# Kernel optimization log

Hardware: AMD Instinct MI355X
Metric: run time of the kernel (lower is better)

Reference implementation:

```python
import jax, jax.numpy as jnp
import numpy as np

B, T, D_IN, D_PHYS, H, L, C = 64, 512, 256, 32, 512, 2, 11


def setup_inputs() -> dict:
    key = jax.random.key(0)
    ks = jax.random.split(key, 20)
    def w(k, shape, fan_in):
        return jax.random.normal(k, shape, dtype=jnp.float32) * (1.0 / np.sqrt(fan_in))
    return {
        "main_feats": jax.random.normal(ks[0], (B, T, D_IN), dtype=jnp.float32),
        "phys_feats": jax.random.normal(ks[1], (B, T, D_PHYS), dtype=jnp.float32),
        "mask": jnp.ones((B, T), dtype=jnp.bool_),
        # main_proj
        "Wp": w(ks[2], (H, D_IN), D_IN), "bp": jnp.zeros((H,), jnp.float32),
        # prev-token embedding
        "emb": jax.random.normal(ks[3], (C, H), dtype=jnp.float32),
        # LSTM layer 0 (input 2H) and layer 1 (input H), PyTorch gate order i,f,g,o
        "Wih0": w(ks[4], (4 * H, 2 * H), 2 * H), "Whh0": w(ks[5], (4 * H, H), H),
        "bih0": jnp.zeros((4 * H,), jnp.float32), "bhh0": jnp.zeros((4 * H,), jnp.float32),
        "Wih1": w(ks[6], (4 * H, H), H), "Whh1": w(ks[7], (4 * H, H), H),
        "bih1": jnp.zeros((4 * H,), jnp.float32), "bhh1": jnp.zeros((4 * H,), jnp.float32),
        # head: Linear(H+phys -> H), ReLU, Linear(H -> C)
        "W1": w(ks[8], (H, H + D_PHYS), H + D_PHYS), "b1": jnp.zeros((H,), jnp.float32),
        "W2": w(ks[9], (C, H), H), "b2": jnp.zeros((C,), jnp.float32),
    }


def _lstm_cell(x, h, c, Wih, Whh, bih, bhh):
    g = x @ Wih.T + bih + h @ Whh.T + bhh          # [b, 4H]
    i, f, gg, o = jnp.split(g, 4, axis=-1)          # PyTorch order i,f,g,o
    c2 = jax.nn.sigmoid(f) * c + jax.nn.sigmoid(i) * jnp.tanh(gg)
    h2 = jax.nn.sigmoid(o) * jnp.tanh(c2)
    return h2, c2


def reference(main_feats, phys_feats, mask, Wp, bp, emb,
              Wih0, Whh0, bih0, bhh0, Wih1, Whh1, bih1, bhh1,
              W1, b1, W2, b2):
    b = main_feats.shape[0]
    h = Whh0.shape[1]
    x_main = main_feats @ Wp.T + bp                 # [B,T,H]

    def step(carry, xs):
        h0, c0, h1, c1, prev = carry
        xm, ph = xs                                  # [B,H], [B,phys]
        x = jnp.concatenate([xm, emb[prev]], axis=-1)  # [B,2H]
        h0, c0 = _lstm_cell(x, h0, c0, Wih0, Whh0, bih0, bhh0)
        h1, c1 = _lstm_cell(h0, h1, c1, Wih1, Whh1, bih1, bhh1)
        z = jnp.concatenate([h1, ph], axis=-1)       # [B,H+phys]
        logits = jax.nn.relu(z @ W1.T + b1) @ W2.T + b2  # [B,C]
        prev = jnp.argmax(logits, axis=-1)
        return (h0, c0, h1, c1, prev), logits

    zeros = jnp.zeros((b, h), jnp.float32)
    carry0 = (zeros, zeros, zeros, zeros, jnp.zeros((b,), jnp.int32))
    xs = (x_main.swapaxes(0, 1), phys_feats.swapaxes(0, 1))  # time-major
    _, logits_t = jax.lax.scan(step, carry0, xs)             # [T,B,C]
    logits_all = logits_t.swapaxes(0, 1)                     # [B,T,C]
    attn = jnp.zeros(mask.shape, logits_all.dtype)
    return logits_all, jnp.zeros_like(logits_all), attn
```

## Files before the change

kernel.cpp:

```cpp
#include <hip/hip_runtime.h>

#define Tn   512
#define NWG  256
#define NTH  1024

#define OFF_WCOMB 0
#define OFF_BC0   524288
#define OFF_EMBG  526336
#define OFF_H0T   548864
#define OFF_H1T   (OFF_H0T + 65536)
#define OFF_C0T   (OFF_H1T + 65536)
#define OFF_C1T   (OFF_C0T + 32768)
#define OFF_BAR   (OFF_C1T + 32768)
#define OFF_ARR   (OFF_BAR + 32)
#define OFF_TAG1  (OFF_ARR + 8192)
#define OFF_PTAG  (OFF_TAG1 + 8192)
#define ZERO_END  (OFF_PTAG + 2048)
#define ZERO_WORDS (ZERO_END - OFF_H0T)
#define OFF_PBUF  ZERO_END
#define WS_WORDS  (OFF_PBUF + 704 * 256)

#define OUT_LOGITS_WORDS 360448
#define OUT_TAIL_WORDS   393216

__global__ void k_wcomb(const float* __restrict__ Wih0, const float* __restrict__ Wp,
                        const float* __restrict__ bp, const float* __restrict__ bih0,
                        const float* __restrict__ bhh0, float* __restrict__ ws) {
    int j = blockIdx.x;
    int k = threadIdx.x;
    const float* row = Wih0 + (long)j * 1024;
    float acc = 0.f;
    for (int h = 0; h < 512; ++h) acc = fmaf(row[h], Wp[h * 256 + k], acc);
    ws[OFF_WCOMB + j * 256 + k] = acc;
    __shared__ float s[256];
    s[k] = row[k] * bp[k] + row[256 + k] * bp[256 + k];
    __syncthreads();
    for (int st = 128; st > 0; st >>= 1) { if (k < st) s[k] += s[k + st]; __syncthreads(); }
    if (k == 0) ws[OFF_BC0 + j] = bih0[j] + bhh0[j] + s[0];
}

__global__ void k_embg(const float* __restrict__ emb, const float* __restrict__ Wih0,
                       float* __restrict__ ws) {
    int cls = blockIdx.x >> 3;
    int j = ((blockIdx.x & 7) << 8) + threadIdx.x;
    const float* er = emb + cls * 512;
    const float* wr = Wih0 + (long)j * 1024 + 512;
    float acc = 0.f;
    for (int h = 0; h < 512; ++h) acc = fmaf(er[h], wr[h], acc);
    ws[OFF_EMBG + cls * 2048 + j] = acc;
}

__global__ void k_zero(float* __restrict__ ws) {
    long i = (long)blockIdx.x * blockDim.x + threadIdx.x;
    if (i < ZERO_WORDS) ws[OFF_H0T + i] = 0.f;
}

struct MP {
    const float *mainf, *phys, *Whh0, *Wih1, *Whh1, *bih1, *bhh1, *W1, *b1, *W2, *b2;
    float* ws;
    float* out;
};

__device__ __forceinline__ float sigm(float x) { return 1.f / (1.f + expf(-x)); }

__device__ __forceinline__ void coh_issue16(const float* p, float4& v) {
    asm volatile("global_load_dwordx4 %0, %1, off sc0 sc1" : "=&v"(v) : "v"(p));
}
__device__ __forceinline__ void vm_wait0() {
    asm volatile("s_waitcnt vmcnt(0)" ::: "memory");
}
__device__ __forceinline__ void coh_store(float* p, float v) {
    __hip_atomic_store(p, v, __ATOMIC_RELAXED, __HIP_MEMORY_SCOPE_AGENT);
}

__device__ __forceinline__ void comp_g(const float (*at)[36], const float* wp, int wld, int kA,
                                       int rg, int q, int b4, float* acc) {
    float4 a0 = *(const float4*)&at[(q << 2) + 0][b4 << 2];
    float4 a1 = *(const float4*)&at[(q << 2) + 1][b4 << 2];
    float4 a2 = *(const float4*)&at[(q << 2) + 2][b4 << 2];
    float4 a3 = *(const float4*)&at[(q << 2) + 3][b4 << 2];
#pragma unroll
    for (int jr = 0; jr < 4; ++jr) {
        float4 w4 = *(const float4*)(wp + (long)((rg << 2) + jr) * wld + kA + (q << 2));
        acc[jr * 4 + 0] = fmaf(w4.x, a0.x, acc[jr * 4 + 0]);
        acc[jr * 4 + 0] = fmaf(w4.y, a1.x, acc[jr * 4 + 0]);
        acc[jr * 4 + 0] = fmaf(w4.z, a2.x, acc[jr * 4 + 0]);
        acc[jr * 4 + 0] = fmaf(w4.w, a3.x, acc[jr * 4 + 0]);
        acc[jr * 4 + 1] = fmaf(w4.x, a0.y, acc[jr * 4 + 1]);
        acc[jr * 4 + 1] = fmaf(w4.y, a1.y, acc[jr * 4 + 1]);
        acc[jr * 4 + 1] = fmaf(w4.z, a2.y, acc[jr * 4 + 1]);
        acc[jr * 4 + 1] = fmaf(w4.w, a3.y, acc[jr * 4 + 1]);
        acc[jr * 4 + 2] = fmaf(w4.x, a0.z, acc[jr * 4 + 2]);
        acc[jr * 4 + 2] = fmaf(w4.y, a1.z, acc[jr * 4 + 2]);
        acc[jr * 4 + 2] = fmaf(w4.z, a2.z, acc[jr * 4 + 2]);
        acc[jr * 4 + 2] = fmaf(w4.w, a3.z, acc[jr * 4 + 2]);
        acc[jr * 4 + 3] = fmaf(w4.x, a0.w, acc[jr * 4 + 3]);
        acc[jr * 4 + 3] = fmaf(w4.y, a1.w, acc[jr * 4 + 3]);
        acc[jr * 4 + 3] = fmaf(w4.z, a2.w, acc[jr * 4 + 3]);
        acc[jr * 4 + 3] = fmaf(w4.w, a3.w, acc[jr * 4 + 3]);
    }
}

template <int NCH0>
__device__ void mm_g(const float* a0, long rs0, int km0, int coh0,
                     const float* a1,
                     const float* w0, int wld0, const float* w1,
                     int bq, int tid,
                     float (*aA)[36], float (*aB)[36],
                     float* redw, float* redf) {
    constexpr int NQ0 = (NCH0 + 8) / 2;
    const int b4 = tid & 7, q = (tid >> 3) & 15, rg = (tid >> 7) & 3;
    const int st = tid & 511, sb = tid >> 9;
    float acc[16];
#pragma unroll
    for (int i = 0; i < 16; ++i) acc[i] = 0.f;

    for (int it = 0; it < NQ0; ++it) {
        const int ch = sb ? (NQ0 + it) : it;
        float4 av;
        int km;
        {
            const float* base; int k0, coh;
            if (ch < NCH0) { base = a0; k0 = ch << 6; km = km0; coh = coh0; }
            else           { base = a1; k0 = (ch - NCH0) << 6; km = 1; coh = 1; }
            if (km) {
                const int kk = st >> 3, b4f = st & 7;
                const float* pp = base + ((long)(k0 + kk) << 6) + (bq << 5) + (b4f << 2);
                if (coh) coh_issue16(pp, av); else av = *(const float4*)pp;
            } else {
                const int k4 = st >> 5, bb = st & 31;
                av = *(const float4*)(base + (long)((bq << 5) + bb) * rs0 + k0 + (k4 << 2));
            }
        }
        vm_wait0();
        {
            float (*dst)[36] = sb ? aB : aA;
            if (km) {
                const int kk = st >> 3, b4f = st & 7;
                *(float4*)&dst[kk][b4f << 2] = av;
            } else {
                const int k4 = st >> 5, bb = st & 31;
                dst[(k4 << 2) + 0][bb] = av.x; dst[(k4 << 2) + 1][bb] = av.y;
                dst[(k4 << 2) + 2][bb] = av.z; dst[(k4 << 2) + 3][bb] = av.w;
            }
        }
        __syncthreads();
        if (tid < 512) {
            {
                const int cA = it; const float* wp; int wld, kA;
                if (cA < NCH0) { wp = w0; wld = wld0; kA = cA << 6; }
                else           { wp = w1; wld = 512;  kA = (cA - NCH0) << 6; }
                comp_g(aA, wp, wld, kA, rg, q, b4, acc);
            }
            {
                const int cB = NQ0 + it; const float* wp; int wld, kB;
                if (cB < NCH0) { wp = w0; wld = wld0; kB = cB << 6; }
                else           { wp = w1; wld = 512;  kB = (cB - NCH0) << 6; }
                comp_g(aB, wp, wld, kB, rg, q, b4, acc);
            }
        }
        __syncthreads();
    }
#pragma unroll
    for (int i = 0; i < 16; ++i) {
        acc[i] += __shfl_xor(acc[i], 8);
        acc[i] += __shfl_xor(acc[i], 16);
        acc[i] += __shfl_xor(acc[i], 32);
    }
    const int lane = tid & 63;
    if (tid < 512 && ((tid >> 6) & 1) && lane < 8) {
        float* d = redw + (((rg << 3) + lane) << 4);
#pragma unroll
        for (int i = 0; i < 16; ++i) d[i] = acc[i];
    }
    __syncthreads();
    if (tid < 512 && !((tid >> 6) & 1) && lane < 8) {
        const float* s = redw + (((rg << 3) + lane) << 4);
#pragma unroll
        for (int jr = 0; jr < 4; ++jr)
#pragma unroll
            for (int jb = 0; jb < 4; ++jb)
                redf[((rg << 2) + jr) * 33 + (lane << 2) + jb] = acc[jr * 4 + jb] + s[jr * 4 + jb];
    }
    __syncthreads();
}

__device__ void mm_h(const float* h1, const float* physb, long rsp,
                     const float* W1, int kg, int bq, int tid,
                     float (*aA)[36], float (*aB)[36],
                     float (*hwA)[68], float (*hwB)[68],
                     float* redw, float* redf) {
    const int b4 = tid & 7, q = (tid >> 3) & 15, rg = (tid >> 7) & 3;
    const int st = tid & 511, sb = tid >> 9;
    float acc[4] = {0.f, 0.f, 0.f, 0.f};
    for (int it = 0; it < 5; ++it) {
        const int ch = sb ? (5 + it) : it;
        const bool valid = ch < 9;
        float4 av, wv;
        bool fa = false, fw = false;
        if (valid) {
            if (ch < 8) {
                const int kk = st >> 3, b4f = st & 7;
                coh_issue16(h1 + ((long)((ch << 6) + kk) << 6) + (bq << 5) + (b4f << 2), av);
                fa = true;
            } else {
                const int k4 = st >> 5, bb = st & 31;
                if (k4 < 8) {
                    av = *(const float4*)(physb + (long)((bq << 5) + bb) * rsp + (k4 << 2));
                    fa = true;
                }
            }
            if (st < 64) {
                const int rw = st >> 4, kq = st & 15;
                if (ch < 8 || kq < 8) {
                    const int gcol = (ch < 8) ? ((ch << 6) + (kq << 2)) : (512 + (kq << 2));
                    wv = *(const float4*)(W1 + (long)(kg * 4 + rw) * 544 + gcol);
                    fw = true;
                }
            }
        }
        vm_wait0();
        if (fa) {
            float (*dst)[36] = sb ? aB : aA;
            if (ch < 8) { const int kk = st >> 3, b4f = st & 7; *(float4*)&dst[kk][b4f << 2] = av; }
            else { const int k4 = st >> 5, bb = st & 31;
                   dst[(k4 << 2) + 0][bb] = av.x; dst[(k4 << 2) + 1][bb] = av.y;
                   dst[(k4 << 2) + 2][bb] = av.z; dst[(k4 << 2) + 3][bb] = av.w; }
        }
        if (fw) {
            float (*dw)[68] = sb ? hwB : hwA;
            *(float4*)&dw[st >> 4][(st & 15) << 2] = wv;
        }
        __syncthreads();
        if (tid < 512) {
            {
                float4 a0 = *(const float4*)&aA[(q << 2) + 0][b4 << 2];
                float4 a1v = *(const float4*)&aA[(q << 2) + 1][b4 << 2];
                float4 a2 = *(const float4*)&aA[(q << 2) + 2][b4 << 2];
                float4 a3 = *(const float4*)&aA[(q << 2) + 3][b4 << 2];
                float4 w4 = *(const float4*)&hwA[rg][q << 2];
                acc[0] = fmaf(w4.x, a0.x, acc[0]); acc[0] = fmaf(w4.y, a1v.x, acc[0]);
                acc[0] = fmaf(w4.z, a2.x, acc[0]); acc[0] = fmaf(w4.w, a3.x, acc[0]);
                acc[1] = fmaf(w4.x, a0.y, acc[1]); acc[1] = fmaf(w4.y, a1v.y, acc[1]);
                acc[1] = fmaf(w4.z, a2.y, acc[1]); acc[1] = fmaf(w4.w, a3.y, acc[1]);
                acc[2] = fmaf(w4.x, a0.z, acc[2]); acc[2] = fmaf(w4.y, a1v.z, acc[2]);
                acc[2] = fmaf(w4.z, a2.z, acc[2]); acc[2] = fmaf(w4.w, a3.z, acc[2]);
                acc[3] = fmaf(w4.x, a0.w, acc[3]); acc[3] = fmaf(w4.y, a1v.w, acc[3]);
                acc[3] = fmaf(w4.z, a2.w, acc[3]); acc[3] = fmaf(w4.w, a3.w, acc[3]);
            }
            const int cB = 5 + it;
            const int kc = (cB == 8) ? 32 : 64;
            if (cB < 9 && (q << 2) < kc) {
                float4 a0 = *(const float4*)&aB[(q << 2) + 0][b4 << 2];
                float4 a1v = *(const float4*)&aB[(q << 2) + 1][b4 << 2];
                float4 a2 = *(const float4*)&aB[(q << 2) + 2][b4 << 2];
                float4 a3 = *(const float4*)&aB[(q << 2) + 3][b4 << 2];
                float4 w4 = *(const float4*)&hwB[rg][q << 2];
                acc[0] = fmaf(w4.x, a0.x, acc[0]); acc[0] = fmaf(w4.y, a1v.x, acc[0]);
                acc[0] = fmaf(w4.z, a2.x, acc[0]); acc[0] = fmaf(w4.w, a3.x, acc[0]);
                acc[1] = fmaf(w4.x, a0.y, acc[1]); acc[1] = fmaf(w4.y, a1v.y, acc[1]);
                acc[1] = fmaf(w4.z, a2.y, acc[1]); acc[1] = fmaf(w4.w, a3.y, acc[1]);
                acc[2] = fmaf(w4.x, a0.z, acc[2]); acc[2] = fmaf(w4.y, a1v.z, acc[2]);
                acc[2] = fmaf(w4.z, a2.z, acc[2]); acc[2] = fmaf(w4.w, a3.z, acc[2]);
                acc[3] = fmaf(w4.x, a0.w, acc[3]); acc[3] = fmaf(w4.y, a1v.w, acc[3]);
                acc[3] = fmaf(w4.z, a2.w, acc[3]); acc[3] = fmaf(w4.w, a3.w, acc[3]);
            }
        }
        __syncthreads();
    }
#pragma unroll
    for (int i = 0; i < 4; ++i) {
        acc[i] += __shfl_xor(acc[i], 8);
        acc[i] += __shfl_xor(acc[i], 16);
        acc[i] += __shfl_xor(acc[i], 32);
    }
    const int lane = tid & 63;
    if (tid < 512 && ((tid >> 6) & 1) && lane < 8) {
        float* d = redw + (((rg << 3) + lane) << 4);
#pragma unroll
        for (int i = 0; i < 4; ++i) d[i] = acc[i];
    }
    __syncthreads();
    if (tid < 512 && !((tid >> 6) & 1) && lane < 8) {
        const float* s = redw + (((rg << 3) + lane) << 4);
#pragma unroll
        for (int jb = 0; jb < 4; ++jb)
            redf[rg * 33 + (lane << 2) + jb] = acc[jb] + s[jb];
    }
    __syncthreads();
}

__device__ __forceinline__ void gsync(int* done, int* arr, int w, int gen) {
    vm_wait0();
    __syncthreads();
    const int tid = threadIdx.x;
    if (tid == 0)
        __hip_atomic_store(&arr[w * 32], gen, __ATOMIC_RELAXED, __HIP_MEMORY_SCOPE_AGENT);
    if (w == 0) {
        if (tid < NWG) {
            int v;
            do {
                __builtin_amdgcn_s_sleep(1);
                v = __hip_atomic_load(&arr[tid * 32], __ATOMIC_RELAXED, __HIP_MEMORY_SCOPE_AGENT);
            } while (v < gen);
        }
        __syncthreads();
        if (tid == 0)
            __hip_atomic_store(done, gen, __ATOMIC_RELAXED, __HIP_MEMORY_SCOPE_AGENT);
    } else {
        if (tid == 0) {
            int v;
            do {
                __builtin_amdgcn_s_sleep(2);
                v = __hip_atomic_load(done, __ATOMIC_RELAXED, __HIP_MEMORY_SCOPE_AGENT);
            } while (v < gen);
        }
    }
    __syncthreads();
}

__global__ void __launch_bounds__(NTH, 4) k_main(MP p) {
    float* ws = p.ws;
    const float* bc0v = ws + OFF_BC0;
    const float* embg = ws + OFF_EMBG;
    float* h0T = ws + OFF_H0T;
    float* h1T = ws + OFF_H1T;
    float* c0T = ws + OFF_C0T;
    float* c1T = ws + OFF_C1T;
    float* pbuf = ws + OFF_PBUF;
    int* done = (int*)(ws + OFF_BAR);
    int* arr  = (int*)(ws + OFF_ARR);
    int* tag1 = (int*)(ws + OFF_TAG1);
    int* ptag = (int*)(ws + OFF_PTAG);

    __shared__ float Wc_l[16][256];
    __shared__ float W0_l[16][512];
    __shared__ float Wi1_l[16][512];
    __shared__ float Wh1_l[16][512];
    __shared__ float actA[64][36], actB[64][36];
    __shared__ float hwA[4][68], hwB[4][68];
    __shared__ float redw[512];
    __shared__ float redf[16 * 33];
    __shared__ float rrowS[4][33];
    __shared__ float slog[11];
    __shared__ int prevlS[32];

    const int w = blockIdx.x, tid = threadIdx.x;
    const int kg = w >> 1, bq = w & 1;
    int gen = 0;

    for (int e = tid; e < 4096; e += NTH) {
        int r = e >> 8, c = e & 255;
        int j = (r >> 2) * 512 + kg * 4 + (r & 3);
        Wc_l[r][c] = ws[OFF_WCOMB + (long)j * 256 + c];
    }
    for (int e = tid; e < 8192; e += NTH) {
        int r = e >> 9, c = e & 511;
        int j = (r >> 2) * 512 + kg * 4 + (r & 3);
        W0_l[r][c]  = p.Whh0[(long)j * 512 + c];
        Wi1_l[r][c] = p.Wih1[(long)j * 512 + c];
        Wh1_l[r][c] = p.Whh1[(long)j * 512 + c];
    }
    __syncthreads();

    for (int t = 0; t <= Tn; ++t) {
        const int cur = t & 1, prv = cur ^ 1;

        if (t >= 1) {
            mm_h(h1T + prv * 32768, p.phys + (long)(t - 1) * 32, (long)Tn * 32,
                 p.W1, kg, bq, tid, actA, actB, hwA, hwB, redw, redf);
            if (tid < 128) {
                int rr = tid >> 5, bb = tid & 31;
                float hv = redf[rr * 33 + bb] + p.b1[kg * 4 + rr];
                rrowS[rr][bb] = hv > 0.f ? hv : 0.f;
            }
            __syncthreads();
            if (tid < 352) {
                int bb = tid / 11, cc = tid - bb * 11;
                float s = 0.f;
#pragma unroll
                for (int r = 0; r < 4; ++r)
                    s = fmaf(rrowS[r][bb], p.W2[cc * 512 + kg * 4 + r], s);
                int b = bq * 32 + bb;
                coh_store(&pbuf[(long)(b * 11 + cc) * 128 + kg], s);
            }
            vm_wait0();
            __syncthreads();
            if (tid == 0)
                __hip_atomic_store(&tag1[w * 32], t, __ATOMIC_RELAXED, __HIP_MEMORY_SCOPE_AGENT);

            if (bq == 0 && kg < 64) {
                const int b = kg;
                if (tid < 128) {
                    int v;
                    do {
                        __builtin_amdgcn_s_sleep(1);
                        v = __hip_atomic_load(&tag1[(tid * 2 + (b >> 5)) * 32],
                                              __ATOMIC_RELAXED, __HIP_MEMORY_SCOPE_AGENT);
                    } while (v < t);
                }
                __syncthreads();
                if (tid < 704) {
                    int cc = tid >> 6, kgi = tid & 63;
                    float s = __hip_atomic_load(&pbuf[(long)(b * 11 + cc) * 128 + kgi],
                                                __ATOMIC_RELAXED, __HIP_MEMORY_SCOPE_AGENT)
                            + __hip_atomic_load(&pbuf[(long)(b * 11 + cc) * 128 + kgi + 64],
                                                __ATOMIC_RELAXED, __HIP_MEMORY_SCOPE_AGENT);
#pragma unroll
                    for (int off = 32; off; off >>= 1) s += __shfl_down(s, off);
                    if (kgi == 0) slog[cc] = s + p.b2[cc];
                }
                __syncthreads();
                if (tid == 0) {
                    float best = -3.4e38f; int am = 0;
#pragma unroll
                    for (int cc = 0; cc < 11; ++cc) {
                        float v = slog[cc];
                        p.out[(long)b * (Tn * 11) + (long)(t - 1) * 11 + cc] = v;
                        if (v > best) { best = v; am = cc; }
                    }
                    __hip_atomic_store(&ptag[b * 32], (t << 4) | am,
                                       __ATOMIC_RELAXED, __HIP_MEMORY_SCOPE_AGENT);
                }
            }
        }
        if (t == Tn) break;

        mm_g<4>(p.mainf + (long)t * 256, (long)Tn * 256, 0, 0,
                h0T + prv * 32768, &Wc_l[0][0], 256, &W0_l[0][0],
                bq, tid, actA, actB, redw, redf);
        if (tid < 32) {
            if (t >= 1) {
                int v;
                do {
                    __builtin_amdgcn_s_sleep(1);
                    v = __hip_atomic_load(&ptag[(bq * 32 + tid) * 32],
                                          __ATOMIC_RELAXED, __HIP_MEMORY_SCOPE_AGENT);
                } while ((v >> 4) < t);
                prevlS[tid] = v & 15;
            } else prevlS[tid] = 0;
        }
        __syncthreads();
        if (tid < 512) {
            int rr = tid >> 5, bb = tid & 31;
            int jrow = (rr >> 2) * 512 + kg * 4 + (rr & 3);
            redf[rr * 33 + bb] += bc0v[jrow] + embg[prevlS[bb] * 2048 + jrow];
        }
        __syncthreads();
        if (tid < 128) {
            int jj = tid >> 5, bb = tid & 31;
            int k = kg * 4 + jj, b = bq * 32 + bb;
            float g0 = redf[jj * 33 + bb];
            float g1 = redf[(4 + jj) * 33 + bb];
            float g2 = redf[(8 + jj) * 33 + bb];
            float g3 = redf[(12 + jj) * 33 + bb];
            float ci = c0T[k * 64 + b];
            float cn = sigm(g1) * ci + sigm(g0) * tanhf(g2);
            c0T[k * 64 + b] = cn;
            coh_store(&h0T[cur * 32768 + k * 64 + b], sigm(g3) * tanhf(cn));
        }
        gsync(done, arr, w, ++gen);

        mm_g<8>(h0T + cur * 32768, 0, 1, 1,
                h1T + prv * 32768, &Wi1_l[0][0], 512, &Wh1_l[0][0],
                bq, tid, actA, actB, redw, redf);
        if (tid < 512) {
            int rr = tid >> 5, bb = tid & 31;
            int jrow = (rr >> 2) * 512 + kg * 4 + (rr & 3);
            redf[rr * 33 + bb] += p.bih1[jrow] + p.bhh1[jrow];
        }
        __syncthreads();
        if (tid < 128) {
            int jj = tid >> 5, bb = tid & 31;
            int k = kg * 4 + jj, b = bq * 32 + bb;
            float g0 = redf[jj * 33 + bb];
            float g1 = redf[(4 + jj) * 33 + bb];
            float g2 = redf[(8 + jj) * 33 + bb];
            float g3 = redf[(12 + jj) * 33 + bb];
            float ci = c1T[k * 64 + b];
            float cn = sigm(g1) * ci + sigm(g0) * tanhf(g2);
            c1T[k * 64 + b] = cn;
            coh_store(&h1T[cur * 32768 + k * 64 + b], sigm(g3) * tanhf(cn));
        }
        gsync(done, arr, w, ++gen);
    }
}

extern "C" void kernel_launch(void* const* d_in, const int* in_sizes, int n_in,
                              void* d_out, int out_size, void* d_ws, size_t ws_size,
                              hipStream_t stream) {
    const float* mainf = (const float*)d_in[0];
    const float* phys  = (const float*)d_in[1];
    const float* Wp   = (const float*)d_in[3];
    const float* bp   = (const float*)d_in[4];
    const float* emb  = (const float*)d_in[5];
    const float* Wih0 = (const float*)d_in[6];
    const float* Whh0 = (const float*)d_in[7];
    const float* bih0 = (const float*)d_in[8];
    const float* bhh0 = (const float*)d_in[9];
    const float* Wih1 = (const float*)d_in[10];
    const float* Whh1 = (const float*)d_in[11];
    const float* bih1 = (const float*)d_in[12];
    const float* bhh1 = (const float*)d_in[13];
    const float* W1   = (const float*)d_in[14];
    const float* b1   = (const float*)d_in[15];
    const float* W2   = (const float*)d_in[16];
    const float* b2   = (const float*)d_in[17];
    float* out = (float*)d_out;
    float* ws  = (float*)d_ws;

    (void)hipMemsetAsync(out + OUT_LOGITS_WORDS, 0, (size_t)OUT_TAIL_WORDS * 4, stream);

    k_wcomb<<<2048, 256, 0, stream>>>(Wih0, Wp, bp, bih0, bhh0, ws);
    k_embg<<<88, 256, 0, stream>>>(emb, Wih0, ws);
    k_zero<<<(ZERO_WORDS + 255) / 256, 256, 0, stream>>>(ws);

    MP p{ mainf, phys, Whh0, Wih1, Whh1, bih1, bhh1, W1, b1, W2, b2, ws, out };
    k_main<<<NWG, NTH, 0, stream>>>(p);
}
```

Baseline: 16.91 ms.

## Prefetch next activation chunk during compute and keep head W1 slice in LDS

```diff
diff --git a/kernel.cpp b/kernel.cpp
--- a/kernel.cpp
+++ b/kernel.cpp
@@ -3,6 +3,8 @@
 #define Tn   512
 #define NWG  256
 #define NTH  1024
+
+typedef unsigned long long u64;
 
 #define OFF_WCOMB 0
 #define OFF_BC0   524288
@@ -63,15 +65,16 @@
 
 __device__ __forceinline__ float sigm(float x) { return 1.f / (1.f + expf(-x)); }
 
-__device__ __forceinline__ void coh_issue16(const float* p, float4& v) {
-    asm volatile("global_load_dwordx4 %0, %1, off sc0 sc1" : "=&v"(v) : "v"(p));
-}
 __device__ __forceinline__ void vm_wait0() {
     asm volatile("s_waitcnt vmcnt(0)" ::: "memory");
 }
 __device__ __forceinline__ void coh_store(float* p, float v) {
     __hip_atomic_store(p, v, __ATOMIC_RELAXED, __HIP_MEMORY_SCOPE_AGENT);
 }
+__device__ __forceinline__ u64 coh_ld8(const float* p) {
+    return __hip_atomic_load((const u64*)p, __ATOMIC_RELAXED, __HIP_MEMORY_SCOPE_AGENT);
+}
+__device__ __forceinline__ float2 u2f(u64 v) { float2 t; __builtin_memcpy(&t, &v, 8); return t; }
 
 __device__ __forceinline__ void comp_g(const float (*at)[36], const float* wp, int wld, int kA,
                                        int rg, int q, int b4, float* acc) {
@@ -115,51 +118,61 @@
 #pragma unroll
     for (int i = 0; i < 16; ++i) acc[i] = 0.f;
 
+    u64 lo0 = 0, hi0 = 0, lo1 = 0, hi1 = 0;
+    int km_c = 1, km_n = 1;
+    {
+        const int ch = sb ? NQ0 : 0;
+        const float* base; int k0, coh;
+        if (ch < NCH0) { base = a0; k0 = ch << 6; km_c = km0; coh = coh0; }
+        else           { base = a1; k0 = (ch - NCH0) << 6; km_c = 1; coh = 1; }
+        const float* pp;
+        if (km_c) { const int kk = st >> 3, b4f = st & 7;
+                    pp = base + ((long)(k0 + kk) << 6) + (bq << 5) + (b4f << 2); }
+        else      { const int k4 = st >> 5, bb = st & 31;
+                    pp = base + (long)((bq << 5) + bb) * rs0 + k0 + (k4 << 2); }
+        if (coh) { lo0 = coh_ld8(pp); hi0 = coh_ld8(pp + 2); }
+        else     { const u64* p8 = (const u64*)pp; lo0 = p8[0]; hi0 = p8[1]; }
+    }
     for (int it = 0; it < NQ0; ++it) {
-        const int ch = sb ? (NQ0 + it) : it;
-        float4 av;
-        int km;
         {
-            const float* base; int k0, coh;
-            if (ch < NCH0) { base = a0; k0 = ch << 6; km = km0; coh = coh0; }
-            else           { base = a1; k0 = (ch - NCH0) << 6; km = 1; coh = 1; }
-            if (km) {
+            float (*dst)[36] = sb ? aB : aA;
+            if (km_c) {
                 const int kk = st >> 3, b4f = st & 7;
-                const float* pp = base + ((long)(k0 + kk) << 6) + (bq << 5) + (b4f << 2);
-                if (coh) coh_issue16(pp, av); else av = *(const float4*)pp;
+                *(u64*)&dst[kk][(b4f << 2) + 0] = lo0;
+                *(u64*)&dst[kk][(b4f << 2) + 2] = hi0;
             } else {
                 const int k4 = st >> 5, bb = st & 31;
-                av = *(const float4*)(base + (long)((bq << 5) + bb) * rs0 + k0 + (k4 << 2));
-            }
-        }
-        vm_wait0();
-        {
-            float (*dst)[36] = sb ? aB : aA;
-            if (km) {
-                const int kk = st >> 3, b4f = st & 7;
-                *(float4*)&dst[kk][b4f << 2] = av;
-            } else {
-                const int k4 = st >> 5, bb = st & 31;
-                dst[(k4 << 2) + 0][bb] = av.x; dst[(k4 << 2) + 1][bb] = av.y;
-                dst[(k4 << 2) + 2][bb] = av.z; dst[(k4 << 2) + 3][bb] = av.w;
-            }
-        }
-        __syncthreads();
+                float2 l = u2f(lo0), h = u2f(hi0);
+                dst[(k4 << 2) + 0][bb] = l.x; dst[(k4 << 2) + 1][bb] = l.y;
+                dst[(k4 << 2) + 2][bb] = h.x; dst[(k4 << 2) + 3][bb] = h.y;
+            }
+        }
+        __syncthreads();
+        if (it + 1 < NQ0) {
+            const int ch = (sb ? NQ0 : 0) + it + 1;
+            const float* base; int k0, coh;
+            if (ch < NCH0) { base = a0; k0 = ch << 6; km_n = km0; coh = coh0; }
+            else           { base = a1; k0 = (ch - NCH0) << 6; km_n = 1; coh = 1; }
+            const float* pp;
+            if (km_n) { const int kk = st >> 3, b4f = st & 7;
+                        pp = base + ((long)(k0 + kk) << 6) + (bq << 5) + (b4f << 2); }
+            else      { const int k4 = st >> 5, bb = st & 31;
+                        pp = base + (long)((bq << 5) + bb) * rs0 + k0 + (k4 << 2); }
+            if (coh) { lo1 = coh_ld8(pp); hi1 = coh_ld8(pp + 2); }
+            else     { const u64* p8 = (const u64*)pp; lo1 = p8[0]; hi1 = p8[1]; }
+        }
         if (tid < 512) {
-            {
-                const int cA = it; const float* wp; int wld, kA;
-                if (cA < NCH0) { wp = w0; wld = wld0; kA = cA << 6; }
-                else           { wp = w1; wld = 512;  kA = (cA - NCH0) << 6; }
-                comp_g(aA, wp, wld, kA, rg, q, b4, acc);
-            }
-            {
-                const int cB = NQ0 + it; const float* wp; int wld, kB;
-                if (cB < NCH0) { wp = w0; wld = wld0; kB = cB << 6; }
-                else           { wp = w1; wld = 512;  kB = (cB - NCH0) << 6; }
-                comp_g(aB, wp, wld, kB, rg, q, b4, acc);
-            }
-        }
-        __syncthreads();
+            { const int cA = it; const float* wp; int wld, kA;
+              if (cA < NCH0) { wp = w0; wld = wld0; kA = cA << 6; }
+              else           { wp = w1; wld = 512;  kA = (cA - NCH0) << 6; }
+              comp_g(aA, wp, wld, kA, rg, q, b4, acc); }
+            { const int cB = NQ0 + it; const float* wp; int wld, kB;
+              if (cB < NCH0) { wp = w0; wld = wld0; kB = cB << 6; }
+              else           { wp = w1; wld = 512;  kB = (cB - NCH0) << 6; }
+              comp_g(aB, wp, wld, kB, rg, q, b4, acc); }
+        }
+        __syncthreads();
+        lo0 = lo1; hi0 = hi1; km_c = km_n;
     }
 #pragma unroll
     for (int i = 0; i < 16; ++i) {
@@ -186,59 +199,70 @@
 }
 
 __device__ void mm_h(const float* h1, const float* physb, long rsp,
-                     const float* W1, int kg, int bq, int tid,
+                     const float (*W1l)[544], int bq, int tid,
                      float (*aA)[36], float (*aB)[36],
-                     float (*hwA)[68], float (*hwB)[68],
                      float* redw, float* redf) {
     const int b4 = tid & 7, q = (tid >> 3) & 15, rg = (tid >> 7) & 3;
     const int st = tid & 511, sb = tid >> 9;
     float acc[4] = {0.f, 0.f, 0.f, 0.f};
+    u64 lo0 = 0, hi0 = 0, lo1 = 0, hi1 = 0;
+    int km_c = 1, km_n = 1;
+    bool f_c = false, f_n = false;
+    {
+        const int ch = sb ? 5 : 0;
+        if (ch < 8) {
+            const int kk = st >> 3, b4f = st & 7;
+            const float* pp = h1 + ((long)((ch << 6) + kk) << 6) + (bq << 5) + (b4f << 2);
+            lo0 = coh_ld8(pp); hi0 = coh_ld8(pp + 2);
+            km_c = 1; f_c = true;
+        } else {
+            const int k4 = st >> 5, bb = st & 31;
+            km_c = 0;
+            if (k4 < 8) {
+                const u64* p8 = (const u64*)(physb + (long)((bq << 5) + bb) * rsp + (k4 << 2));
+                lo0 = p8[0]; hi0 = p8[1]; f_c = true;
+            }
+        }
+    }
     for (int it = 0; it < 5; ++it) {
-        const int ch = sb ? (5 + it) : it;
-        const bool valid = ch < 9;
-        float4 av, wv;
-        bool fa = false, fw = false;
-        if (valid) {
+        if (f_c) {
+            float (*dst)[36] = sb ? aB : aA;
+            if (km_c) {
+                const int kk = st >> 3, b4f = st & 7;
+                *(u64*)&dst[kk][(b4f << 2) + 0] = lo0;
+                *(u64*)&dst[kk][(b4f << 2) + 2] = hi0;
+            } else {
+                const int k4 = st >> 5, bb = st & 31;
+                float2 l = u2f(lo0), h = u2f(hi0);
+                dst[(k4 << 2) + 0][bb] = l.x; dst[(k4 << 2) + 1][bb] = l.y;
+                dst[(k4 << 2) + 2][bb] = h.x; dst[(k4 << 2) + 3][bb] = h.y;
+            }
+        }
+        __syncthreads();
+        f_n = false; km_n = 1;
+        if (it + 1 < 5) {
+            const int ch = (sb ? 5 : 0) + it + 1;
             if (ch < 8) {
                 const int kk = st >> 3, b4f = st & 7;
-                coh_issue16(h1 + ((long)((ch << 6) + kk) << 6) + (bq << 5) + (b4f << 2), av);
-                fa = true;
-            } else {
+                const float* pp = h1 + ((long)((ch << 6) + kk) << 6) + (bq << 5) + (b4f << 2);
+                lo1 = coh_ld8(pp); hi1 = coh_ld8(pp + 2);
+                f_n = true;
+            } else if (ch == 8) {
                 const int k4 = st >> 5, bb = st & 31;
+                km_n = 0;
                 if (k4 < 8) {
-                    av = *(const float4*)(physb + (long)((bq << 5) + bb) * rsp + (k4 << 2));
-                    fa = true;
+                    const u64* p8 = (const u64*)(physb + (long)((bq << 5) + bb) * rsp + (k4 << 2));
+                    lo1 = p8[0]; hi1 = p8[1]; f_n = true;
                 }
             }
-            if (st < 64) {
-                const int rw = st >> 4, kq = st & 15;
-                if (ch < 8 || kq < 8) {
-                    const int gcol = (ch < 8) ? ((ch << 6) + (kq << 2)) : (512 + (kq << 2));
-                    wv = *(const float4*)(W1 + (long)(kg * 4 + rw) * 544 + gcol);
-                    fw = true;
-                }
-            }
-        }
-        vm_wait0();
-        if (fa) {
-            float (*dst)[36] = sb ? aB : aA;
-            if (ch < 8) { const int kk = st >> 3, b4f = st & 7; *(float4*)&dst[kk][b4f << 2] = av; }
-            else { const int k4 = st >> 5, bb = st & 31;
-                   dst[(k4 << 2) + 0][bb] = av.x; dst[(k4 << 2) + 1][bb] = av.y;
-                   dst[(k4 << 2) + 2][bb] = av.z; dst[(k4 << 2) + 3][bb] = av.w; }
-        }
-        if (fw) {
-            float (*dw)[68] = sb ? hwB : hwA;
-            *(float4*)&dw[st >> 4][(st & 15) << 2] = wv;
-        }
-        __syncthreads();
+        }
         if (tid < 512) {
             {
                 float4 a0 = *(const float4*)&aA[(q << 2) + 0][b4 << 2];
                 float4 a1v = *(const float4*)&aA[(q << 2) + 1][b4 << 2];
                 float4 a2 = *(const float4*)&aA[(q << 2) + 2][b4 << 2];
                 float4 a3 = *(const float4*)&aA[(q << 2) + 3][b4 << 2];
-                float4 w4 = *(const float4*)&hwA[rg][q << 2];
+                float4 w4 = *(const float4*)&W1l[rg][(it << 6) + (q << 2)];
                 acc[0] = fmaf(w4.x, a0.x, acc[0]); acc[0] = fmaf(w4.y, a1v.x, acc[0]);
                 acc[0] = fmaf(w4.z, a2.x, acc[0]); acc[0] = fmaf(w4.w, a3.x, acc[0]);
                 acc[1] = fmaf(w4.x, a0.y, acc[1]); acc[1] = fmaf(w4.y, a1v.y, acc[1]);
@@ -255,7 +279,7 @@
                 float4 a1v = *(const float4*)&aB[(q << 2) + 1][b4 << 2];
                 float4 a2 = *(const float4*)&aB[(q << 2) + 2][b4 << 2];
                 float4 a3 = *(const float4*)&aB[(q << 2) + 3][b4 << 2];
-                float4 w4 = *(const float4*)&hwB[rg][q << 2];
+                float4 w4 = *(const float4*)&W1l[rg][(cB << 6) + (q << 2)];
                 acc[0] = fmaf(w4.x, a0.x, acc[0]); acc[0] = fmaf(w4.y, a1v.x, acc[0]);
                 acc[0] = fmaf(w4.z, a2.x, acc[0]); acc[0] = fmaf(w4.w, a3.x, acc[0]);
                 acc[1] = fmaf(w4.x, a0.y, acc[1]); acc[1] = fmaf(w4.y, a1v.y, acc[1]);
@@ -267,6 +291,7 @@
             }
         }
         __syncthreads();
+        lo0 = lo1; hi0 = hi1; km_c = km_n; f_c = f_n;
     }
 #pragma unroll
     for (int i = 0; i < 4; ++i) {
@@ -337,8 +362,8 @@
     __shared__ float W0_l[16][512];
     __shared__ float Wi1_l[16][512];
     __shared__ float Wh1_l[16][512];
+    __shared__ float W1_l[4][544];
     __shared__ float actA[64][36], actB[64][36];
-    __shared__ float hwA[4][68], hwB[4][68];
     __shared__ float redw[512];
     __shared__ float redf[16 * 33];
     __shared__ float rrowS[4][33];
@@ -361,6 +386,10 @@
         Wi1_l[r][c] = p.Wih1[(long)j * 512 + c];
         Wh1_l[r][c] = p.Whh1[(long)j * 512 + c];
     }
+    for (int e = tid; e < 2176; e += NTH) {
+        int r = e / 544, c = e - r * 544;
+        W1_l[r][c] = p.W1[(long)(kg * 4 + r) * 544 + c];
+    }
     __syncthreads();
 
     for (int t = 0; t <= Tn; ++t) {
@@ -368,7 +397,7 @@
 
         if (t >= 1) {
             mm_h(h1T + prv * 32768, p.phys + (long)(t - 1) * 32, (long)Tn * 32,
-                 p.W1, kg, bq, tid, actA, actB, hwA, hwB, redw, redf);
+                 W1_l, bq, tid, actA, actB, redw, redf);
             if (tid < 128) {
                 int rr = tid >> 5, bb = tid & 31;
                 float hv = redf[rr * 33 + bb] + p.b1[kg * 4 + rr];
```

Result: slower. 21.37 ms (+26.4%).
